# Optimization experiments

Hardware: AMD Instinct MI355X
Metric: run time of the kernel (lower is better)

## Reference

```python
import jax, jax.numpy as jnp
import numpy as np

B, S, D, H, RANK, NC = 2, 2048, 1024, 16, 128, 16
DH = D // H


def setup_inputs() -> dict:
    key = jax.random.key(0)
    ks = jax.random.split(key, 10)
    x = jax.random.normal(ks[0], (B, S, D), jnp.float32)
    # causal mask, broadcast over batch and heads like torch's [B,1,S,S]
    mask = jnp.tril(jnp.ones((S, S), dtype=bool))[None, None]
    # orthogonal-ish init approximated by scaled gaussian
    compress_neurons = jax.random.normal(ks[1], (NC, D, RANK), jnp.float32) / np.sqrt(D)
    router_Q = jax.random.normal(ks[2], (NC, D), jnp.float32) * 0.02
    router_K = jax.random.normal(ks[3], (NC, D), jnp.float32) * 0.02
    router_V = jax.random.normal(ks[4], (NC, D), jnp.float32) * 0.02
    wQ = jax.random.normal(ks[5], (D, RANK), jnp.float32) / np.sqrt(RANK)
    wK = jax.random.normal(ks[6], (D, RANK), jnp.float32) / np.sqrt(RANK)
    wV = jax.random.normal(ks[7], (D, RANK), jnp.float32) / np.sqrt(RANK)
    wO = jax.random.normal(ks[8], (D, D), jnp.float32) / np.sqrt(D)
    return {"x": x, "mask": mask, "compress_neurons": compress_neurons,
            "router_Q": router_Q, "router_K": router_K, "router_V": router_V,
            "wQ": wQ, "wK": wK, "wV": wV, "wO": wO}


def reference(x, mask, compress_neurons, router_Q, router_K, router_V, wQ, wK, wV, wO):
    def compress(router_w):
        # router scores -> softmax over all n_compress neurons
        w = jax.nn.softmax(jnp.einsum('bsd,nd->bsn', x, router_w), axis=-1)  # [B,S,NC]
        # softmax-weighted sum of all neuron projections (fused einsum)
        return jnp.einsum('bsd,ndr,bsn->bsr', x, compress_neurons, w)  # [B,S,RANK]

    hQ = compress(router_Q)
    hK = compress(router_K)
    hV = compress(router_V)
    # expand rank -> d_model (Linear weight [D,RANK]), then split heads
    Q = jnp.einsum('bsr,dr->bsd', hQ, wQ).reshape(B, S, H, DH).transpose(0, 2, 1, 3)
    K = jnp.einsum('bsr,dr->bsd', hK, wK).reshape(B, S, H, DH).transpose(0, 2, 1, 3)
    V = jnp.einsum('bsr,dr->bsd', hV, wV).reshape(B, S, H, DH).transpose(0, 2, 1, 3)
    scores = jnp.einsum('bhqd,bhkd->bhqk', Q, K) / np.sqrt(DH)  # [B,H,S,S]
    scores = jnp.where(mask, scores, -jnp.inf)
    attn = jax.nn.softmax(scores, axis=-1)
    attn_out = jnp.einsum('bhqk,bhkd->bhqd', attn, V)
    attn_out = attn_out.transpose(0, 2, 1, 3).reshape(B, S, D)
    # dropout omitted (eval mode / dropout=0)
    return jnp.einsum('bsd,ed->bse', attn_out, wO)
```

## Files before the change

### kernel.cpp

```cpp
#include <hip/hip_runtime.h>
#include <hip/hip_bf16.h>
#include <math.h>

#define B_ 2
#define S_ 2048
#define D_ 1024
#define H_ 16
#define RANK_ 128
#define NC_ 16
#define DH_ 64
#define T_ (B_*S_)
#define NZ_ 2176

typedef __attribute__((ext_vector_type(8))) __bf16 bf16x8;
typedef __attribute__((ext_vector_type(8))) unsigned short u16x8;
typedef __attribute__((ext_vector_type(4))) float f32x4;
typedef __attribute__((ext_vector_type(16))) float f32x16;

#if __has_builtin(__builtin_amdgcn_exp2f)
#define EXP2F(x) __builtin_amdgcn_exp2f(x)
#else
#define EXP2F(x) exp2f(x)
#endif

__device__ __forceinline__ unsigned short f2bu(float f) {
    __hip_bfloat16 h = __float2bfloat16(f);
    unsigned short u; __builtin_memcpy(&u, &h, 2); return u;
}
__device__ __forceinline__ float bu2f(unsigned short u) {
    __hip_bfloat16 h; __builtin_memcpy(&h, &u, 2); return __bfloat162float(h);
}

__device__ __forceinline__ void gl_lds16(const unsigned short* g, unsigned short* l) {
    __builtin_amdgcn_global_load_lds(
        (const __attribute__((address_space(1))) void*)g,
        (__attribute__((address_space(3))) void*)l, 16, 0, 0);
}

__device__ __forceinline__ unsigned cvtpk_bf16(float lo, float hi) {
    unsigned r;
    asm("v_cvt_pk_bf16_f32 %0, %1, %2" : "=v"(r) : "v"(lo), "v"(hi));
    return r;
}
__device__ __forceinline__ void plswap(unsigned &a, unsigned &b) {
    asm("v_permlane32_swap_b32 %0, %1" : "+v"(a), "+v"(b));
}

__device__ __forceinline__ bool sniff_f32(const unsigned* __restrict__ p) {
    int votes = 0;
    #pragma unroll
    for (int i = 0; i < 64; i++) {
        unsigned e = (p[i] >> 23) & 0xFFu;
        votes += (e >= 0x60u && e <= 0x8Fu) ? 1 : 0;
    }
    return votes >= 32;
}

struct Cvt { const void* src[9]; unsigned short* dst[9]; const void* C; unsigned short* Ct; };

__global__ __launch_bounds__(256) void k_inputs(Cvt cv,
    const unsigned* __restrict__ probe)
{
    bool f32 = sniff_f32(probe);
    if (blockIdx.x < 512) {
        int bid = blockIdx.x;
        int d0 = (bid & 15) * 64, r0 = ((bid >> 4) & 1) * 64, n = bid >> 5;
        __shared__ unsigned short tile[64][65];
        for (int idx = threadIdx.x; idx < 4096; idx += 256) {
            int row = idx >> 6, col = idx & 63;
            size_t si = ((size_t)n*D_ + d0 + row)*RANK_ + r0 + col;
            tile[row][col] = f32 ? f2bu(((const float*)cv.C)[si])
                                 : ((const unsigned short*)cv.C)[si];
        }
        __syncthreads();
        for (int idx = threadIdx.x; idx < 4096; idx += 256) {
            int row = idx >> 6, col = idx & 63;
            cv.Ct[((size_t)(n*RANK_ + r0 + row))*D_ + d0 + col] = tile[col][row];
        }
        return;
    }
    const int offs[9] = {0, 4194304, 4210688, 4227072, 4243456,
                         4259840, 4390912, 4521984, 4653056};
    const int total = 5701632;
    int nconv = gridDim.x - 512;
    int stride = nconv * 256;
    for (int i = (blockIdx.x - 512) * 256 + threadIdx.x; i < total; i += stride) {
        int seg = 0;
        #pragma unroll
        for (int s = 1; s < 9; s++) seg += (i >= offs[s]) ? 1 : 0;
        int local = i - offs[seg];
        const void* sp = cv.src[seg];
        unsigned short v = 0;
        if (sp) v = f32 ? f2bu(((const float*)sp)[local]) : ((const unsigned short*)sp)[local];
        cv.dst[seg][local] = v;
    }
}

template<int MT, int MODE>
__global__ __launch_bounds__(256) void k_mfma_gemm(const unsigned short* __restrict__ A,
    const unsigned short* __restrict__ Bm, void* __restrict__ Cout,
    const unsigned* __restrict__ probe, int M, int N, int K)
{
    bool f32out = false;
    if (MODE == 2) f32out = sniff_f32(probe);
    __shared__ __align__(16) unsigned short As[MT*32*32];
    __shared__ __align__(16) unsigned short Bs[128*32];
    const int tid = threadIdx.x;
    const int wv = tid >> 6, lane = tid & 63;
    const int wm = (wv >> 1) * (MT*16), wn = (wv & 1) * 64;
    const int quad = lane >> 4, l16 = lane & 15;
    const int m0 = blockIdx.x * (MT*32), n0 = blockIdx.y * 128;

    const f32x4 z4 = {0.f, 0.f, 0.f, 0.f};
    f32x4 acc[MT][4];
    #pragma unroll
    for (int i = 0; i < MT; i++)
        #pragma unroll
        for (int j = 0; j < 4; j++) acc[i][j] = z4;

    for (int k0 = 0; k0 < K; k0 += 32) {
        __syncthreads();
        #pragma unroll
        for (int c = 0; c < MT/2; c++) {
            int idx = wv*64 + c*256 + lane;
            gl_lds16(A + (size_t)(m0 + (idx >> 2))*K + k0 + (idx & 3)*8,
                     &As[(wv*64 + c*256)*8]);
        }
        #pragma unroll
        for (int c = 0; c < 2; c++) {
            int idx = wv*64 + c*256 + lane;
            gl_lds16(Bm + (size_t)(n0 + (idx >> 2))*K + k0 + (idx & 3)*8,
                     &Bs[(wv*64 + c*256)*8]);
        }
        __syncthreads();
        bf16x8 af[MT], bfr[4];
        #pragma unroll
        for (int mt = 0; mt < MT; mt++) af[mt]  = *(const bf16x8*)&As[(wm + mt*16 + l16)*32 + quad*8];
        #pragma unroll
        for (int nt = 0; nt < 4; nt++) bfr[nt] = *(const bf16x8*)&Bs[(wn + nt*16 + l16)*32 + quad*8];
        #pragma unroll
        for (int mt = 0; mt < MT; mt++)
            #pragma unroll
            for (int nt = 0; nt < 4; nt++)
                acc[mt][nt] = __builtin_amdgcn_mfma_f32_16x16x32_bf16(af[mt], bfr[nt], acc[mt][nt], 0, 0, 0);
    }
    #pragma unroll
    for (int mt = 0; mt < MT; mt++)
        #pragma unroll
        for (int nt = 0; nt < 4; nt++) {
            int col = n0 + wn + nt*16 + l16;
            #pragma unroll
            for (int r = 0; r < 4; r++) {
                int rowg = m0 + wm + mt*16 + quad*4 + r;
                float v = acc[mt][nt][r];
                if (MODE == 2 && f32out) ((float*)Cout)[(size_t)rowg*N + col] = v;
                else  ((unsigned short*)Cout)[(size_t)rowg*N + col] = f2bu(v);
            }
        }
}

__global__ __launch_bounds__(256) void k_qkv2(const unsigned short* __restrict__ h3,
    const unsigned short* __restrict__ wqkv, unsigned short* __restrict__ QKb,
    unsigned short* __restrict__ Vtg)
{
    __shared__ __align__(16) unsigned short As[128*32];
    __shared__ __align__(16) unsigned short Bs[128*32];
    const int tid = threadIdx.x;
    const int wv = tid >> 6, lane = tid & 63;
    const int wm = (wv >> 1) * 64, wn = (wv & 1) * 64;
    const int quad = lane >> 4, l16 = lane & 15;

    const bool vt = (blockIdx.x >= 512);
    int m0, n0;
    const unsigned short *A, *Bm;
    float scale = 1.f;
    if (!vt) {
        int id = blockIdx.x;
        m0 = (id & 31) * 128;
        n0 = (id >> 5) * 128;
        int w = n0 >> 10;
        A  = h3 + (size_t)w * T_ * RANK_ + (size_t)m0 * RANK_;
        Bm = wqkv + (size_t)w * D_ * RANK_ + (size_t)(n0 & 1023) * RANK_;
        if (w == 0) scale = 0.125f * 1.44269504f;
    } else {
        int id = blockIdx.x - 512;
        m0 = (id & 7) * 128;
        n0 = (id >> 3) * 128;
        A  = wqkv + (size_t)2 * D_ * RANK_ + (size_t)m0 * RANK_;
        Bm = h3 + (size_t)2 * T_ * RANK_ + (size_t)n0 * RANK_;
    }

    const f32x4 z4 = {0.f, 0.f, 0.f, 0.f};
    f32x4 acc[4][4];
    #pragma unroll
    for (int i = 0; i < 4; i++)
        #pragma unroll
        for (int j = 0; j < 4; j++) acc[i][j] = z4;

    for (int k0 = 0; k0 < RANK_; k0 += 32) {
        __syncthreads();
        #pragma unroll
        for (int c = 0; c < 2; c++) {
            int idx = wv*64 + c*256 + lane;
            gl_lds16(A  + (size_t)(idx >> 2)*RANK_ + k0 + (idx & 3)*8,
                     &As[(wv*64 + c*256)*8]);
            gl_lds16(Bm + (size_t)(idx >> 2)*RANK_ + k0 + (idx & 3)*8,
                     &Bs[(wv*64 + c*256)*8]);
        }
        __syncthreads();
        bf16x8 af[4], bfr[4];
        #pragma unroll
        for (int mt = 0; mt < 4; mt++) af[mt]  = *(const bf16x8*)&As[(wm + mt*16 + l16)*32 + quad*8];
        #pragma unroll
        for (int nt = 0; nt < 4; nt++) bfr[nt] = *(const bf16x8*)&Bs[(wn + nt*16 + l16)*32 + quad*8];
        #pragma unroll
        for (int mt = 0; mt < 4; mt++)
            #pragma unroll
            for (int nt = 0; nt < 4; nt++)
                acc[mt][nt] = __builtin_amdgcn_mfma_f32_16x16x32_bf16(af[mt], bfr[nt], acc[mt][nt], 0, 0, 0);
    }
    #pragma unroll
    for (int mt = 0; mt < 4; mt++)
        #pragma unroll
        for (int nt = 0; nt < 4; nt++) {
            #pragma unroll
            for (int r = 0; r < 4; r++) {
                int rowg = m0 + wm + mt*16 + quad*4 + r;
                int col  = n0 + wn + nt*16 + l16;
                float v = acc[mt][nt][r] * scale;
                if (!vt) {
                    QKb[(size_t)(col >> 10)*T_*D_ + (size_t)rowg*D_ + (col & 1023)]
                        = f2bu(v);
                } else {
                    size_t vrow = (size_t)((col >> 11)*H_ + (rowg >> 6))*64 + (rowg & 63);
                    Vtg[vrow*S_ + (col & 2047)] = f2bu(v);
                }
            }
        }
}

__global__ __launch_bounds__(256) void k_hreduce(const unsigned short* __restrict__ z,
    unsigned short* __restrict__ h)
{
    int t0 = blockIdx.x * 2;
    int tg = threadIdx.x >> 7, r = threadIdx.x & 127;
    int t = t0 + tg;
    __shared__ float sc[2][48];
    __shared__ float wl[2][3][16];
    if (threadIdx.x < 96) {
        int tk = threadIdx.x / 48, j = threadIdx.x % 48;
        sc[tk][j] = bu2f(z[(size_t)(t0 + tk)*NZ_ + 2048 + j]);
    }
    __syncthreads();
    if (threadIdx.x < 6) {
        int tk = threadIdx.x / 3, w = threadIdx.x % 3;
        float m = -INFINITY;
        for (int n = 0; n < 16; n++) m = fmaxf(m, sc[tk][w*16 + n]);
        float s = 0.f, e[16];
        for (int n = 0; n < 16; n++) { e[n] = __expf(sc[tk][w*16 + n] - m); s += e[n]; }
        float inv = 1.f / s;
        for (int n = 0; n < 16; n++) wl[tk][w][n] = e[n] * inv;
    }
    __syncthreads();
    const unsigned short* zr = z + (size_t)t * NZ_;
    float acc[3] = {0.f, 0.f, 0.f};
    #pragma unroll
    for (int n = 0; n < NC_; n++) {
        float zv = bu2f(zr[n*RANK_ + r]);
        #pragma unroll
        for (int w = 0; w < 3; w++) acc[w] += wl[tg][w][n] * zv;
    }
    #pragma unroll
    for (int w = 0; w < 3; w++) h[((size_t)w*T_ + t)*RANK_ + r] = f2bu(acc[w]);
}

__global__ __launch_bounds__(256, 2) void k_flash_mfma(const unsigned short* __restrict__ Qm,
    const unsigned short* __restrict__ Km, const unsigned short* __restrict__ Vtg,
    unsigned short* __restrict__ Om)
{
    const int i = blockIdx.x;
    const int half = i >> 8, r_ = i & 255;
    const int gr = r_ & 31, ts = r_ >> 5;
    const int qt = half ? ts : (15 - ts);
    const int hh = gr & 15, b = gr >> 4;

    __shared__ __align__(16) unsigned short Ks[2][64*64];
    __shared__ __align__(16) unsigned short Vs[2][64*64];
    const int tid = threadIdx.x;
    const int w = tid >> 6, lane = tid & 63;
    const int l32 = lane & 31, hi = lane >> 5;
    const size_t base  = ((size_t)b * S_) * D_ + (size_t)hh * DH_;
    const size_t vbase = (size_t)((b*H_ + hh) * 64) * S_;
    const int tokg = qt*128 + w*32 + l32;

    bf16x8 aq[4];
    #pragma unroll
    for (int ks = 0; ks < 4; ks++)
        aq[ks] = *(const bf16x8*)(Qm + base + (size_t)tokg*D_ + ks*16 + hi*8);

    f32x16 oacc[2];
    #pragma unroll
    for (int db = 0; db < 2; db++)
        #pragma unroll
        for (int ii = 0; ii < 16; ii++) oacc[db][ii] = 0.f;
    float lsum = 0.f;

    const int nkt = 2*(qt + 1);

    #pragma unroll
    for (int c = 0; c < 2; c++) {
        int idx = c*256 + tid;
        int row = idx >> 3, j = (idx & 7) ^ (row & 7);
        gl_lds16(Km + base + (size_t)row*D_ + j*8, &Ks[0][(c*256 + (w<<6))*8]);
    }
    #pragma unroll
    for (int c = 0; c < 2; c++) {
        int idx = c*256 + tid;
        int row = idx >> 3, j = (idx & 7) ^ (row & 7);
        gl_lds16(Vtg + vbase + (size_t)row*S_ + j*8, &Vs[0][(c*256 + (w<<6))*8]);
    }

    for (int kt = 0; kt < nkt; kt++) {
        const int cur = kt & 1;
        __syncthreads();

        if (kt + 1 < nkt) {
            #pragma unroll
            for (int c = 0; c < 2; c++) {
                int idx = c*256 + tid;
                int row = idx >> 3, j = (idx & 7) ^ (row & 7);
                gl_lds16(Km + base + (size_t)((kt+1)*64 + row)*D_ + j*8,
                         &Ks[1-cur][(c*256 + (w<<6))*8]);
            }
            #pragma unroll
            for (int c = 0; c < 2; c++) {
                int idx = c*256 + tid;
                int row = idx >> 3, j = (idx & 7) ^ (row & 7);
                gl_lds16(Vtg + vbase + (size_t)row*S_ + (kt+1)*64 + j*8,
                         &Vs[1-cur][(c*256 + (w<<6))*8]);
            }
        }

        f32x16 sacc[2];
        #pragma unroll
        for (int kb = 0; kb < 2; kb++)
            #pragma unroll
            for (int ii = 0; ii < 16; ii++) sacc[kb][ii] = 0.f;
        #pragma unroll
        for (int ks = 0; ks < 4; ks++)
            #pragma unroll
            for (int kb = 0; kb < 2; kb++) {
                int row = kb*32 + l32;
                int c = (ks*2 + hi) ^ (row & 7);
                bf16x8 ak = *(const bf16x8*)&Ks[cur][row*64 + c*8];
                sacc[kb] = __builtin_amdgcn_mfma_f32_32x32x16_bf16(ak, aq[ks], sacc[kb], 0, 0, 0);
            }

        if (kt >= 2*qt) {
            #pragma unroll
            for (int kb = 0; kb < 2; kb++)
                #pragma unroll
                for (int r = 0; r < 16; r++) {
                    int keyg = kt*64 + kb*32 + (r&3) + 8*(r>>2) + 4*hi;
                    if (keyg > tokg) sacc[kb][r] = -INFINITY;
                }
        }

        bf16x8 pa[4];
        #pragma unroll
        for (int kb = 0; kb < 2; kb++) {
            float pv[16];
            #pragma unroll
            for (int r = 0; r < 16; r++) {
                pv[r] = EXP2F(sacc[kb][r]);
                lsum += pv[r];
            }
            unsigned wd[8];
            #pragma unroll
            for (int j = 0; j < 8; j++) wd[j] = cvtpk_bf16(pv[2*j], pv[2*j+1]);
            plswap(wd[0], wd[2]); plswap(wd[1], wd[3]);
            plswap(wd[4], wd[6]); plswap(wd[5], wd[7]);
            union { unsigned u[4]; bf16x8 v; } u0, u1;
            u0.u[0]=wd[0]; u0.u[1]=wd[1]; u0.u[2]=wd[2]; u0.u[3]=wd[3];
            u1.u[0]=wd[4]; u1.u[1]=wd[5]; u1.u[2]=wd[6]; u1.u[3]=wd[7];
            pa[2*kb]   = u0.v;
            pa[2*kb+1] = u1.v;
        }

        #pragma unroll
        for (int ks = 0; ks < 4; ks++)
            #pragma unroll
            for (int db = 0; db < 2; db++) {
                int row = db*32 + l32;
                int c = (ks*2 + hi) ^ (row & 7);
                bf16x8 bv = *(const bf16x8*)&Vs[cur][row*64 + c*8];
                oacc[db] = __builtin_amdgcn_mfma_f32_32x32x16_bf16(pa[ks], bv, oacc[db], 0, 0, 0);
            }
    }

    float l = lsum + __shfl_xor(lsum, 32);
    float inv = 1.f / l;
    #pragma unroll
    for (int r = 0; r < 16; r++) {
        int crow = (r&3) + 8*(r>>2) + 4*hi;
        float invr = __shfl(inv, crow);
        size_t rowo = base + (size_t)(qt*128 + w*32 + crow)*D_;
        #pragma unroll
        for (int db = 0; db < 2; db++)
            Om[rowo + db*32 + l32] = f2bu(oacc[db][r] * invr);
    }
}

extern "C" void kernel_launch(void* const* d_in, const int* in_sizes, int n_in,
                              void* d_out, int out_size, void* d_ws, size_t ws_size,
                              hipStream_t stream)
{
    const unsigned* probe = (const unsigned*)d_in[0];

    unsigned short* u = (unsigned short*)d_ws;
    unsigned short* xc   = u;               size_t o = (size_t)T_*D_;
    unsigned short* wqkv = u + o;           o += (size_t)3*D_*RANK_;
    unsigned short* wOc  = u + o;           o += (size_t)D_*D_;
    unsigned short* Ct   = u + o;           o += (size_t)NZ_*D_;
    unsigned short* h3   = u + o;           o += (size_t)3*T_*RANK_;
    unsigned short* QKb  = u + o;           o += (size_t)2*T_*D_;
    unsigned short* Vtg  = u + o;           o += (size_t)T_*D_;
    unsigned short* z    = u + o;           o += (size_t)T_*NZ_;
    unsigned short* attnb= u + o;           o += (size_t)T_*D_;

    unsigned short* Rp = Ct + (size_t)2048*D_;
    unsigned short* Qb = QKb;
    unsigned short* Kb = QKb + (size_t)T_*D_;

    Cvt cv;
    cv.src[0] = d_in[0]; cv.dst[0] = xc;
    cv.src[1] = d_in[3]; cv.dst[1] = Rp;
    cv.src[2] = d_in[4]; cv.dst[2] = Rp + 16384;
    cv.src[3] = d_in[5]; cv.dst[3] = Rp + 32768;
    cv.src[4] = nullptr; cv.dst[4] = Rp + 49152;
    cv.src[5] = d_in[6]; cv.dst[5] = wqkv;
    cv.src[6] = d_in[7]; cv.dst[6] = wqkv + 131072;
    cv.src[7] = d_in[8]; cv.dst[7] = wqkv + 262144;
    cv.src[8] = d_in[9]; cv.dst[8] = wOc;
    cv.C = d_in[2]; cv.Ct = Ct;
    k_inputs<<<512 + 2048, 256, 0, stream>>>(cv, probe);

    k_mfma_gemm<4,0><<<dim3(T_/128, NZ_/128), 256, 0, stream>>>(
        xc, Ct, z, nullptr, T_, NZ_, D_);

    k_hreduce<<<T_/2, 256, 0, stream>>>(z, h3);

    k_qkv2<<<768, 256, 0, stream>>>(h3, wqkv, QKb, Vtg);

    k_flash_mfma<<<dim3(512), 256, 0, stream>>>(Qb, Kb, Vtg, attnb);

    k_mfma_gemm<2,2><<<dim3(T_/64, D_/128), 256, 0, stream>>>(
        attnb, wOc, d_out, probe, T_, D_, D_);
}
```

Baseline: 229.5 us.

## Split causal attention KV range across blocks with fp32 partials and merge kernel

```diff
diff --git a/kernel.cpp b/kernel.cpp
--- a/kernel.cpp
+++ b/kernel.cpp
@@ -274,15 +274,23 @@
     for (int w = 0; w < 3; w++) h[((size_t)w*T_ + t)*RANK_ + r] = f2bu(acc[w]);
 }
 
-__global__ __launch_bounds__(256, 2) void k_flash_mfma(const unsigned short* __restrict__ Qm,
+__global__ __launch_bounds__(256, 5) void k_flash_mfma(const unsigned short* __restrict__ Qm,
     const unsigned short* __restrict__ Km, const unsigned short* __restrict__ Vtg,
-    unsigned short* __restrict__ Om)
+    float* __restrict__ Op, float* __restrict__ lp)
 {
     const int i = blockIdx.x;
-    const int half = i >> 8, r_ = i & 255;
-    const int gr = r_ & 31, ts = r_ >> 5;
-    const int qt = half ? ts : (15 - ts);
+    const int gr = i & 31, u = i >> 5;
+    int qt, jj;
+    if (u < 16)      { qt = 15 - (u >> 2);          jj = u & 3; }
+    else if (u < 28) { int v = u - 16; qt = 11 - v/3; jj = v - (11 - qt)*3; }
+    else if (u < 36) { int v = u - 28; qt = 7 - (v >> 1); jj = v & 1; }
+    else             { qt = 3 - (u - 36);           jj = 0; }
     const int hh = gr & 15, b = gr >> 4;
+    const int ns = (2*qt + 9) >> 3;
+    const int nall = 2*(qt + 1);
+    const int q_ = nall / ns, rem = nall - q_*ns;
+    const int n = q_ + (jj < rem ? 1 : 0);
+    const int kt0 = jj*q_ + (jj < rem ? jj : rem);
 
     __shared__ __align__(16) unsigned short Ks[2][64*64];
     __shared__ __align__(16) unsigned short Vs[2][64*64];
@@ -305,26 +313,27 @@
         for (int ii = 0; ii < 16; ii++) oacc[db][ii] = 0.f;
     float lsum = 0.f;
 
-    const int nkt = 2*(qt + 1);
-
     #pragma unroll
     for (int c = 0; c < 2; c++) {
         int idx = c*256 + tid;
         int row = idx >> 3, j = (idx & 7) ^ (row & 7);
-        gl_lds16(Km + base + (size_t)row*D_ + j*8, &Ks[0][(c*256 + (w<<6))*8]);
+        gl_lds16(Km + base + (size_t)(kt0*64 + row)*D_ + j*8,
+                 &Ks[0][(c*256 + (w<<6))*8]);
     }
     #pragma unroll
     for (int c = 0; c < 2; c++) {
         int idx = c*256 + tid;
         int row = idx >> 3, j = (idx & 7) ^ (row & 7);
-        gl_lds16(Vtg + vbase + (size_t)row*S_ + j*8, &Vs[0][(c*256 + (w<<6))*8]);
-    }
-
-    for (int kt = 0; kt < nkt; kt++) {
-        const int cur = kt & 1;
+        gl_lds16(Vtg + vbase + (size_t)row*S_ + kt0*64 + j*8,
+                 &Vs[0][(c*256 + (w<<6))*8]);
+    }
+
+    for (int t = 0; t < n; t++) {
+        const int kt = kt0 + t;
+        const int cur = t & 1;
         __syncthreads();
 
-        if (kt + 1 < nkt) {
+        if (t + 1 < n) {
             #pragma unroll
             for (int c = 0; c < 2; c++) {
                 int idx = c*256 + tid;
@@ -346,6 +355,7 @@
         for (int kb = 0; kb < 2; kb++)
             #pragma unroll
             for (int ii = 0; ii < 16; ii++) sacc[kb][ii] = 0.f;
+        __builtin_amdgcn_s_setprio(1);
         #pragma unroll
         for (int ks = 0; ks < 4; ks++)
             #pragma unroll
@@ -355,6 +365,7 @@
                 bf16x8 ak = *(const bf16x8*)&Ks[cur][row*64 + c*8];
                 sacc[kb] = __builtin_amdgcn_mfma_f32_32x32x16_bf16(ak, aq[ks], sacc[kb], 0, 0, 0);
             }
+        __builtin_amdgcn_s_setprio(0);
 
         if (kt >= 2*qt) {
             #pragma unroll
@@ -387,6 +398,7 @@
             pa[2*kb+1] = u1.v;
         }
 
+        __builtin_amdgcn_s_setprio(1);
         #pragma unroll
         for (int ks = 0; ks < 4; ks++)
             #pragma unroll
@@ -396,19 +408,48 @@
                 bf16x8 bv = *(const bf16x8*)&Vs[cur][row*64 + c*8];
                 oacc[db] = __builtin_amdgcn_mfma_f32_32x32x16_bf16(pa[ks], bv, oacc[db], 0, 0, 0);
             }
+        __builtin_amdgcn_s_setprio(0);
     }
 
     float l = lsum + __shfl_xor(lsum, 32);
-    float inv = 1.f / l;
+    if (hi == 0)
+        lp[((size_t)(jj*B_ + b)*H_ + hh)*S_ + qt*128 + w*32 + l32] = l;
+    float* Ob = Op + (size_t)jj * T_ * D_;
     #pragma unroll
     for (int r = 0; r < 16; r++) {
         int crow = (r&3) + 8*(r>>2) + 4*hi;
-        float invr = __shfl(inv, crow);
         size_t rowo = base + (size_t)(qt*128 + w*32 + crow)*D_;
         #pragma unroll
         for (int db = 0; db < 2; db++)
-            Om[rowo + db*32 + l32] = f2bu(oacc[db][r] * invr);
-    }
+            Ob[rowo + db*32 + l32] = oacc[db][r];
+    }
+}
+
+__global__ __launch_bounds__(256) void k_merge(const float* __restrict__ Op,
+    const float* __restrict__ lp, unsigned short* __restrict__ attnb)
+{
+    const size_t i = ((size_t)blockIdx.x * 256 + threadIdx.x) * 8;
+    const int tf = (int)(i >> 10);
+    const int d0 = (int)(i & 1023);
+    const int h = d0 >> 6;
+    const int b = tf >> 11, tok = tf & (S_-1);
+    const int qt = tok >> 7;
+    const int ns = (2*qt + 9) >> 3;
+    float a[8] = {0,0,0,0,0,0,0,0};
+    float l = 0.f;
+    for (int jj = 0; jj < ns; jj++) {
+        const float* O = Op + (size_t)jj * T_ * D_;
+        f32x4 a0 = *(const f32x4*)(O + i);
+        f32x4 a1 = *(const f32x4*)(O + i + 4);
+        #pragma unroll
+        for (int j = 0; j < 4; j++) { a[j] += a0[j]; a[4+j] += a1[j]; }
+        l += lp[((size_t)(jj*B_ + b)*H_ + h)*S_ + tok];
+    }
+    float inv = 1.f / l;
+    u16x8 o8;
+    #pragma unroll
+    for (int j = 0; j < 8; j++) o8[j] = f2bu(a[j] * inv);
+    *(u16x8*)(attnb + i) = o8;
 }
 
 extern "C" void kernel_launch(void* const* d_in, const int* in_sizes, int n_in,
@@ -427,6 +468,8 @@
     unsigned short* Vtg  = u + o;           o += (size_t)T_*D_;
     unsigned short* z    = u + o;           o += (size_t)T_*NZ_;
     unsigned short* attnb= u + o;           o += (size_t)T_*D_;
+    float* Opart = (float*)(u + o);         o += (size_t)8*T_*D_;
+    float* lpart = (float*)(u + o);         o += (size_t)8*B_*H_*S_;
 
     unsigned short* Rp = Ct + (size_t)2048*D_;
     unsigned short* Qb = QKb;
@@ -452,7 +495,9 @@
 
     k_qkv2<<<768, 256, 0, stream>>>(h3, wqkv, QKb, Vtg);
 
-    k_flash_mfma<<<dim3(512), 256, 0, stream>>>(Qb, Kb, Vtg, attnb);
+    k_flash_mfma<<<dim3(1280), 256, 0, stream>>>(Qb, Kb, Vtg, Opart, lpart);
+
+    k_merge<<<dim3(T_*D_/2048), 256, 0, stream>>>(Opart, lpart, attnb);
 
     k_mfma_gemm<2,2><<<dim3(T_/64, D_/128), 256, 0, stream>>>(
         attnb, wOc, d_out, probe, T_, D_, D_);
```

After: 253.1 us. 10.3% more time.
